# Kernel optimization log

Measured on AMD Instinct MI355X. Metric: run time of the kernel, lower is better.

## Reference

```python
import jax, jax.numpy as jnp
import numpy as np

N_EMBD = 2048
N_HEAD = 16
HEAD_DIM = N_EMBD // N_HEAD
BATCH = 2
SEQ = 2048


def setup_inputs() -> dict:
    key = jax.random.key(0)
    k1, k2, k3 = jax.random.split(key, 3)
    scale = 0.02
    return {
        "hidden_states": jax.random.normal(k1, (BATCH, SEQ, N_EMBD), dtype=jnp.float32),
        "c_attn_w": jax.random.normal(k2, (N_EMBD, 3 * N_EMBD), dtype=jnp.float32) * scale,
        "c_attn_b": jnp.zeros((3 * N_EMBD,), dtype=jnp.float32),
        "c_proj_w": jax.random.normal(k3, (N_EMBD, N_EMBD), dtype=jnp.float32) * scale,
        "c_proj_b": jnp.zeros((N_EMBD,), dtype=jnp.float32),
    }


def reference(hidden_states, c_attn_w, c_attn_b, c_proj_w, c_proj_b):
    B, S, E = hidden_states.shape
    # Fused QKV projection (Conv1D: x @ W + b)
    qkv = hidden_states @ c_attn_w + c_attn_b  # [B, S, 3E]
    q, k, v = jnp.split(qkv, 3, axis=-1)
    # split heads -> [B, H, S, D]
    def split_heads(t):
        return t.reshape(B, S, N_HEAD, HEAD_DIM).transpose(0, 2, 1, 3)
    q, k, v = split_heads(q), split_heads(k), split_heads(v)
    # scaled scores, causal mask, softmax (dropout p=0 -> identity)
    scores = jnp.einsum("bhqd,bhkd->bhqk", q, k) / jnp.asarray(
        HEAD_DIM ** 0.5, dtype=q.dtype)
    causal = jnp.tril(jnp.ones((S, S), dtype=bool))  # [S, S]
    mask_value = jnp.finfo(scores.dtype).min
    scores = jnp.where(causal[None, None, :, :], scores, mask_value)
    attn = jax.nn.softmax(scores, axis=-1)
    out = jnp.einsum("bhqk,bhkd->bhqd", attn, v)  # [B, H, S, D]
    # merge heads -> [B, S, E]
    out = out.transpose(0, 2, 1, 3).reshape(B, S, E)
    # output projection
    return out @ c_proj_w + c_proj_b
```

## Files before the change

### kernel.cpp

```cpp
#include <hip/hip_runtime.h>
#include <hip/hip_bf16.h>

typedef __bf16 bf16x8 __attribute__((ext_vector_type(8)));
typedef float f32x4 __attribute__((ext_vector_type(4)));
typedef unsigned short us4 __attribute__((ext_vector_type(4)));
typedef unsigned short us8 __attribute__((ext_vector_type(8)));

__device__ __forceinline__ float bf2f(unsigned short u) {
  union { unsigned int i; float f; } v; v.i = ((unsigned int)u) << 16; return v.f;
}
__device__ __forceinline__ unsigned short f2bf(float f) {
  union { unsigned int i; float f; } v; v.f = f;
  unsigned int i = v.i;
  return (unsigned short)((i + 0x7FFFu + ((i >> 16) & 1u)) >> 16);
}

typedef const __attribute__((address_space(1))) unsigned int* gas_ptr;
typedef __attribute__((address_space(3))) unsigned int* las_ptr;
__device__ __forceinline__ void gload_lds16(const unsigned short* g, unsigned short* l) {
  __builtin_amdgcn_global_load_lds((gas_ptr)(const void*)g, (las_ptr)(void*)l, 16, 0, 0);
}

__global__ __launch_bounds__(256) void detect_k(const unsigned short* __restrict__ h,
                                                int* __restrict__ flag) {
  __shared__ int s[256];
  int cnt = 0;
  for (int i = threadIdx.x; i < 4096; i += 256) {
    unsigned short u = h[2 * i];
    int e = (u >> 7) & 0xFF;
    if ((e >= 96 && e <= 140) || u == 0) cnt++;
  }
  s[threadIdx.x] = cnt;
  __syncthreads();
  for (int o = 128; o > 0; o >>= 1) {
    if (threadIdx.x < o) s[threadIdx.x] += s[threadIdx.x + o];
    __syncthreads();
  }
  if (threadIdx.x == 0) *flag = (s[0] >= 3600) ? 1 : 0;
}

__global__ __launch_bounds__(256) void cvt_hidden_k(const void* __restrict__ src,
                                                    unsigned short* __restrict__ dst, int n8,
                                                    const int* __restrict__ flag) {
  if (*flag) return;
  const float4* s = (const float4*)src;
  for (int i = blockIdx.x * 256 + threadIdx.x; i < n8; i += gridDim.x * 256) {
    float4 a = s[2 * i], b = s[2 * i + 1];
    us8 o;
    o[0] = f2bf(a.x); o[1] = f2bf(a.y); o[2] = f2bf(a.z); o[3] = f2bf(a.w);
    o[4] = f2bf(b.x); o[5] = f2bf(b.y); o[6] = f2bf(b.z); o[7] = f2bf(b.w);
    *(us8*)&dst[8 * i] = o;
  }
}

__global__ __launch_bounds__(256) void transpose_w2_k(const void* __restrict__ w_qkv,
                                                      const void* __restrict__ w_proj,
                                                      unsigned short* __restrict__ dst_qkv,
                                                      unsigned short* __restrict__ dst_proj,
                                                      const int* __restrict__ flag) {
  __shared__ unsigned short tile[32][33];
  const int f = *flag;
  int bid = blockIdx.x;
  const void* src;
  unsigned short* dst;
  int R = 2048, C, cx, cy;
  if (bid < 12288) {
    src = w_qkv; dst = dst_qkv; C = 6144; cx = bid % 192; cy = bid / 192;
  } else {
    bid -= 12288;
    src = w_proj; dst = dst_proj; C = 2048; cx = bid % 64; cy = bid / 64;
  }
  const int x = threadIdx.x & 31;
  const int y = threadIdx.x >> 5;
  const int r0 = cy * 32, c0 = cx * 32;
#pragma unroll
  for (int i = 0; i < 4; i++) {
    size_t idx = (size_t)(r0 + y + 8 * i) * C + c0 + x;
    tile[y + 8 * i][x] = f ? ((const unsigned short*)src)[idx]
                           : f2bf(((const float*)src)[idx]);
  }
  __syncthreads();
  const int orow = threadIdx.x >> 3;
  const int oc = (threadIdx.x & 7) * 4;
  us4 v;
  v[0] = tile[oc][orow]; v[1] = tile[oc + 1][orow];
  v[2] = tile[oc + 2][orow]; v[3] = tile[oc + 3][orow];
  *(us4*)&dst[(size_t)(c0 + orow) * R + r0 + oc] = v;
}

__global__ __launch_bounds__(256) void transpose_v_k(const unsigned short* __restrict__ qkv,
                                                     unsigned short* __restrict__ Vt) {
  __shared__ unsigned short tile[32][33];
  const int bh = blockIdx.z;
  const int b = bh >> 4, hh = bh & 15;
  const int s0 = blockIdx.x * 32, d0 = blockIdx.y * 32;
  const int x = threadIdx.x & 31, y = threadIdx.x >> 5;
#pragma unroll
  for (int i = 0; i < 4; i++)
    tile[y + 8 * i][x] =
        qkv[((size_t)b * 2048 + s0 + y + 8 * i) * 6144 + 4096 + hh * 128 + d0 + x];
  __syncthreads();
#pragma unroll
  for (int i = 0; i < 4; i++)
    Vt[((size_t)bh * 128 + d0 + y + 8 * i) * 2048 + s0 + x] = tile[x][y + 8 * i];
}

__global__ __launch_bounds__(512, 2) void gemm_qkv_k(const unsigned short* __restrict__ A_bf,
                                                     const unsigned short* __restrict__ A_cvt,
                                                     const unsigned short* __restrict__ Bt,
                                                     const void* __restrict__ bias,
                                                     unsigned short* __restrict__ Cout,
                                                     int M, int N, int K,
                                                     const int* __restrict__ flag) {
  __shared__ __attribute__((aligned(16))) unsigned short As[2][256][64];
  __shared__ __attribute__((aligned(16))) unsigned short Bs[2][192][64];
  const int f = *flag;
  const unsigned short* Ap = f ? A_bf : A_cvt;
  const int t = threadIdx.x;
  const int wave = t >> 6, lane = t & 63;
  const int col = lane & 15, quad = lane >> 4;
  const int wm = wave >> 1, wn = wave & 1;

  const int nbx = N / 192;
  int wgid = blockIdx.y * nbx + blockIdx.x;
  const int nwg = (M >> 8) * nbx;
  if ((nwg & 7) == 0) {
    const int cpx = nwg >> 3;
    wgid = (wgid & 7) * cpx + (wgid >> 3);
  }
  const int n0 = (wgid % nbx) * 192;
  const int m0 = (wgid / nbx) << 8;

  const int srow = lane >> 3;
  const int sx = ((lane & 7) ^ srow) * 8;
  const int rsw = col & 7;

  const unsigned short* pA = Ap + (size_t)(m0 + wave * 8 + srow) * K + sx;
  const unsigned short* pB = Bt + (size_t)(n0 + wave * 8 + srow) * K + sx;
  const int NT = K >> 6;

#define STAGE_A(d, q, kt) \
  gload_lds16(pA + (size_t)((q) * 64) * K + (size_t)(kt) * 64, &As[(d)][(q) * 64 + wave * 8][0])
#define STAGE_B(d, q, kt) \
  gload_lds16(pB + (size_t)((q) * 64) * K + (size_t)(kt) * 64, &Bs[(d)][(q) * 64 + wave * 8][0])
#define LDA(d, rf, kk) \
  (*(const bf16x8*)&As[(d)][wm * 64 + (rf) * 16 + col][((((kk) << 2) | quad) ^ rsw) * 8])
#define LDB(d, cf, kk) \
  (*(const bf16x8*)&Bs[(d)][wn * 96 + (cf) * 16 + col][((((kk) << 2) | quad) ^ rsw) * 8])

  const f32x4 fzero = {0.f, 0.f, 0.f, 0.f};
  f32x4 acc[4][6];
#pragma unroll
  for (int i = 0; i < 4; i++)
#pragma unroll
    for (int j = 0; j < 6; j++) acc[i][j] = fzero;

  bf16x8 aA[4][2], aB[4][2];

  STAGE_A(0, 0, 0); STAGE_A(0, 1, 0); STAGE_A(0, 2, 0); STAGE_A(0, 3, 0);
  STAGE_B(0, 0, 0); STAGE_B(0, 1, 0); STAGE_B(0, 2, 0);
  STAGE_A(1, 0, 1); STAGE_A(1, 1, 1); STAGE_A(1, 2, 1); STAGE_A(1, 3, 1);
  asm volatile("s_waitcnt vmcnt(4)" ::: "memory");
  __builtin_amdgcn_sched_barrier(0);
  __builtin_amdgcn_s_barrier();

#define BODY(D, U, FIRST, SB, SA, VM2, VM3, PRER, ACUR, ANXT)                              \
  {                                                                                        \
    if (FIRST) {                                                                           \
      _Pragma("unroll") for (int rf = 0; rf < 4; rf++) {                                   \
        ACUR[rf][0] = LDA(D, rf, 0);                                                       \
        ACUR[rf][1] = LDA(D, rf, 1);                                                       \
      }                                                                                    \
    }                                                                                      \
    bf16x8 b01[2][2];                                                                      \
    _Pragma("unroll") for (int c = 0; c < 2; c++) {                                        \
      b01[c][0] = LDB(D, c, 0);                                                            \
      b01[c][1] = LDB(D, c, 1);                                                            \
    }                                                                                      \
    if (SB) { STAGE_B((D) ^ 1, 0, (U) + 1); STAGE_B((D) ^ 1, 1, (U) + 1); }                \
    __builtin_amdgcn_s_barrier();                                                          \
    asm volatile("s_waitcnt lgkmcnt(0)" ::: "memory");                                     \
    __builtin_amdgcn_sched_barrier(0);                                                     \
    __builtin_amdgcn_s_setprio(1);                                                         \
    _Pragma("unroll") for (int rf = 0; rf < 4; rf++)                                       \
      _Pragma("unroll") for (int c = 0; c < 2; c++) {                                      \
        acc[rf][c] = __builtin_amdgcn_mfma_f32_16x16x32_bf16(ACUR[rf][0], b01[c][0], acc[rf][c], 0, 0, 0); \
        acc[rf][c] = __builtin_amdgcn_mfma_f32_16x16x32_bf16(ACUR[rf][1], b01[c][1], acc[rf][c], 0, 0, 0); \
      }                                                                                    \
    __builtin_amdgcn_s_setprio(0);                                                         \
    bf16x8 b23[2][2];                                                                      \
    _Pragma("unroll") for (int c = 0; c < 2; c++) {                                        \
      b23[c][0] = LDB(D, (c) + 2, 0);                                                      \
      b23[c][1] = LDB(D, (c) + 2, 1);                                                      \
    }                                                                                      \
    if (SB) STAGE_B((D) ^ 1, 2, (U) + 1);                                                  \
    if (SA) { STAGE_A(D, 0, (U) + 2); STAGE_A(D, 1, (U) + 2); }                            \
    asm volatile("s_waitcnt " VM2 ::: "memory");                                           \
    __builtin_amdgcn_s_barrier();                                                          \
    asm volatile("s_waitcnt lgkmcnt(0)" ::: "memory");                                     \
    __builtin_amdgcn_sched_barrier(0);                                                     \
    __builtin_amdgcn_s_setprio(1);                                                         \
    _Pragma("unroll") for (int rf = 0; rf < 4; rf++)                                       \
      _Pragma("unroll") for (int c = 0; c < 2; c++) {                                      \
        acc[rf][(c) + 2] = __builtin_amdgcn_mfma_f32_16x16x32_bf16(ACUR[rf][0], b23[c][0], acc[rf][(c) + 2], 0, 0, 0); \
        acc[rf][(c) + 2] = __builtin_amdgcn_mfma_f32_16x16x32_bf16(ACUR[rf][1], b23[c][1], acc[rf][(c) + 2], 0, 0, 0); \
      }                                                                                    \
    __builtin_amdgcn_s_setprio(0);                                                         \
    bf16x8 b45[2][2];                                                                      \
    _Pragma("unroll") for (int c = 0; c < 2; c++) {                                        \
      b45[c][0] = LDB(D, (c) + 4, 0);                                                      \
      b45[c][1] = LDB(D, (c) + 4, 1);                                                      \
    }                                                                                      \
    __builtin_amdgcn_sched_barrier(0);  \
    if (PRER) {                                                                            \
      _Pragma("unroll") for (int rf = 0; rf < 4; rf++) {                                   \
        ANXT[rf][0] = LDA((D) ^ 1, rf, 0);                                                 \
        ANXT[rf][1] = LDA((D) ^ 1, rf, 1);                                                 \
      }                                                                                    \
    }                                                                                      \
    if (SA) { STAGE_A(D, 2, (U) + 2); STAGE_A(D, 3, (U) + 2); }                            \
    asm volatile("s_waitcnt " VM3 ::: "memory");                                           \
    __builtin_amdgcn_s_barrier();                                                          \
    if (PRER) asm volatile("s_waitcnt lgkmcnt(8)" ::: "memory");                           \
    else      asm volatile("s_waitcnt lgkmcnt(0)" ::: "memory");                           \
    __builtin_amdgcn_sched_barrier(0);                                                     \
    __builtin_amdgcn_s_setprio(1);                                                         \
    _Pragma("unroll") for (int rf = 0; rf < 4; rf++)                                       \
      _Pragma("unroll") for (int c = 0; c < 2; c++) {                                      \
        acc[rf][(c) + 4] = __builtin_amdgcn_mfma_f32_16x16x32_bf16(ACUR[rf][0], b45[c][0], acc[rf][(c) + 4], 0, 0, 0); \
        acc[rf][(c) + 4] = __builtin_amdgcn_mfma_f32_16x16x32_bf16(ACUR[rf][1], b45[c][1], acc[rf][(c) + 4], 0, 0, 0); \
      }                                                                                    \
    __builtin_amdgcn_s_setprio(0);                                                         \
  }

  BODY(0, 0, 1, 1, 1, "vmcnt(5)", "vmcnt(4)", 1, aA, aB)
  BODY(1, 1, 0, 1, 1, "vmcnt(5)", "vmcnt(4)", 1, aB, aA)
  for (int u2 = 2; u2 + 3 < NT; u2 += 2) {
    BODY(0, u2, 0, 1, 1, "vmcnt(5)", "vmcnt(4)", 1, aA, aB)
    BODY(1, u2 + 1, 0, 1, 1, "vmcnt(5)", "vmcnt(4)", 1, aB, aA)
  }
  BODY(0, NT - 2, 0, 1, 0, "vmcnt(3)", "vmcnt(0)", 1, aA, aB)
  BODY(1, NT - 1, 0, 0, 0, "vmcnt(0)", "vmcnt(0)", 0, aB, aA)

#undef BODY
#undef STAGE_A
#undef STAGE_B
#undef LDA
#undef LDB

#pragma unroll
  for (int cf = 0; cf < 6; cf++) {
    int n = n0 + wn * 96 + cf * 16 + col;
    float bv = f ? bf2f(((const unsigned short*)bias)[n]) : ((const float*)bias)[n];
#pragma unroll
    for (int rf = 0; rf < 4; rf++)
#pragma unroll
      for (int r = 0; r < 4; r++) {
        int m = m0 + wm * 64 + rf * 16 + quad * 4 + r;
        Cout[(size_t)m * N + n] = f2bf(acc[rf][cf][r] + bv);
      }
  }
}

__global__ __launch_bounds__(512, 2) void gemm_proj_k(const unsigned short* __restrict__ A,
                                                      const unsigned short* __restrict__ Bt,
                                                      const void* __restrict__ bias,
                                                      void* __restrict__ Cout,
                                                      int M, int N, int K,
                                                      const int* __restrict__ flag) {
  __shared__ __attribute__((aligned(16))) unsigned short As[2][256][64];
  __shared__ __attribute__((aligned(16))) unsigned short Bs[2][128][64];
  const int f = *flag;
  const int t = threadIdx.x;
  const int wave = t >> 6, lane = t & 63;
  const int col = lane & 15, quad = lane >> 4;
  const int wm = wave >> 1, wn = wave & 1;

  const int nbx = N >> 7;
  int wgid = blockIdx.y * nbx + blockIdx.x;
  const int nwg = (M >> 8) * nbx;
  if ((nwg & 7) == 0) {
    const int cpx = nwg >> 3;
    wgid = (wgid & 7) * cpx + (wgid >> 3);
  }
  const int n0 = (wgid % nbx) << 7;
  const int m0 = (wgid / nbx) << 8;

  const int srow = lane >> 3;
  const int sx = ((lane & 7) ^ srow) * 8;
  const int rsw = col & 7;

  const unsigned short* pA = A + (size_t)(m0 + wave * 8 + srow) * K + sx;
  const unsigned short* pB = Bt + (size_t)(n0 + wave * 8 + srow) * K + sx;
  const int NT = K >> 6;

#define STAGE_A(d, q, kt) \
  gload_lds16(pA + (size_t)((q) * 64) * K + (size_t)(kt) * 64, &As[(d)][(q) * 64 + wave * 8][0])
#define STAGE_B(d, q, kt) \
  gload_lds16(pB + (size_t)((q) * 64) * K + (size_t)(kt) * 64, &Bs[(d)][(q) * 64 + wave * 8][0])
#define LDA(d, rf, kk) \
  (*(const bf16x8*)&As[(d)][wm * 64 + (rf) * 16 + col][((((kk) << 2) | quad) ^ rsw) * 8])
#define LDB(d, cf, kk) \
  (*(const bf16x8*)&Bs[(d)][wn * 64 + (cf) * 16 + col][((((kk) << 2) | quad) ^ rsw) * 8])

  const f32x4 fzero = {0.f, 0.f, 0.f, 0.f};
  f32x4 acc[4][4];
#pragma unroll
  for (int i = 0; i < 4; i++)
#pragma unroll
    for (int j = 0; j < 4; j++) acc[i][j] = fzero;

  bf16x8 aA[4][2], aB[4][2];

  STAGE_A(0, 0, 0); STAGE_A(0, 1, 0); STAGE_A(0, 2, 0); STAGE_A(0, 3, 0);
  STAGE_B(0, 0, 0); STAGE_B(0, 1, 0);
  STAGE_A(1, 0, 1); STAGE_A(1, 1, 1); STAGE_A(1, 2, 1); STAGE_A(1, 3, 1);
  asm volatile("s_waitcnt vmcnt(4)" ::: "memory");
  __builtin_amdgcn_sched_barrier(0);
  __builtin_amdgcn_s_barrier();

#define BODY(D, U, FIRST, SB, SA, VM1, VM2, PRER, ACUR, ANXT)                              \
  {                                                                                        \
    if (FIRST) {                                                                           \
      _Pragma("unroll") for (int rf = 0; rf < 4; rf++) {                                   \
        ACUR[rf][0] = LDA(D, rf, 0);                                                       \
        ACUR[rf][1] = LDA(D, rf, 1);                                                       \
      }                                                                                    \
    }                                                                                      \
    bf16x8 b01[2][2];                                                                      \
    _Pragma("unroll") for (int c = 0; c < 2; c++) {                                        \
      b01[c][0] = LDB(D, c, 0);                                                            \
      b01[c][1] = LDB(D, c, 1);                                                            \
    }                                                                                      \
    if (SB) { STAGE_B((D) ^ 1, 0, (U) + 1); STAGE_B((D) ^ 1, 1, (U) + 1); }                \
    asm volatile("s_waitcnt " VM1 ::: "memory");                                           \
    __builtin_amdgcn_s_barrier();                                                          \
    asm volatile("s_waitcnt lgkmcnt(0)" ::: "memory");                                     \
    __builtin_amdgcn_sched_barrier(0);                                                     \
    __builtin_amdgcn_s_setprio(1);                                                         \
    _Pragma("unroll") for (int rf = 0; rf < 4; rf++)                                       \
      _Pragma("unroll") for (int c = 0; c < 2; c++) {                                      \
        acc[rf][c] = __builtin_amdgcn_mfma_f32_16x16x32_bf16(ACUR[rf][0], b01[c][0], acc[rf][c], 0, 0, 0); \
        acc[rf][c] = __builtin_amdgcn_mfma_f32_16x16x32_bf16(ACUR[rf][1], b01[c][1], acc[rf][c], 0, 0, 0); \
      }                                                                                    \
    __builtin_amdgcn_s_setprio(0);                                                         \
    bf16x8 b23[2][2];                                                                      \
    _Pragma("unroll") for (int c = 0; c < 2; c++) {                                        \
      b23[c][0] = LDB(D, (c) + 2, 0);                                                      \
      b23[c][1] = LDB(D, (c) + 2, 1);                                                      \
    }                                                                                      \
    __builtin_amdgcn_sched_barrier(0);                      \
    if (PRER) {                                                                            \
      _Pragma("unroll") for (int rf = 0; rf < 4; rf++) {                                   \
        ANXT[rf][0] = LDA((D) ^ 1, rf, 0);                                                 \
        ANXT[rf][1] = LDA((D) ^ 1, rf, 1);                                                 \
      }                                                                                    \
    }                                                                                      \
    if (SA) { STAGE_A(D, 0, (U) + 2); STAGE_A(D, 1, (U) + 2);                              \
              STAGE_A(D, 2, (U) + 2); STAGE_A(D, 3, (U) + 2); }                            \
    asm volatile("s_waitcnt " VM2 ::: "memory");                                           \
    __builtin_amdgcn_s_barrier();                                                          \
    if (PRER) asm volatile("s_waitcnt lgkmcnt(8)" ::: "memory");                           \
    else      asm volatile("s_waitcnt lgkmcnt(0)" ::: "memory");                           \
    __builtin_amdgcn_sched_barrier(0);                                                     \
    __builtin_amdgcn_s_setprio(1);                                                         \
    _Pragma("unroll") for (int rf = 0; rf < 4; rf++)                                       \
      _Pragma("unroll") for (int c = 0; c < 2; c++) {                                      \
        acc[rf][(c) + 2] = __builtin_amdgcn_mfma_f32_16x16x32_bf16(ACUR[rf][0], b23[c][0], acc[rf][(c) + 2], 0, 0, 0); \
        acc[rf][(c) + 2] = __builtin_amdgcn_mfma_f32_16x16x32_bf16(ACUR[rf][1], b23[c][1], acc[rf][(c) + 2], 0, 0, 0); \
      }                                                                                    \
    __builtin_amdgcn_s_setprio(0);                                                         \
  }

  BODY(0, 0, 1, 1, 1, "vmcnt(2)", "vmcnt(4)", 1, aA, aB)
  BODY(1, 1, 0, 1, 1, "vmcnt(2)", "vmcnt(4)", 1, aB, aA)
  for (int u2 = 2; u2 + 3 < NT; u2 += 2) {
    BODY(0, u2, 0, 1, 1, "vmcnt(2)", "vmcnt(4)", 1, aA, aB)
    BODY(1, u2 + 1, 0, 1, 1, "vmcnt(2)", "vmcnt(4)", 1, aB, aA)
  }
  BODY(0, NT - 2, 0, 1, 0, "vmcnt(2)", "vmcnt(0)", 1, aA, aB)
  BODY(1, NT - 1, 0, 0, 0, "vmcnt(0)", "vmcnt(0)", 0, aB, aA)

#undef BODY
#undef STAGE_A
#undef STAGE_B
#undef LDA
#undef LDB

  const int f32o = (f == 0);
#pragma unroll
  for (int cf = 0; cf < 4; cf++) {
    int n = n0 + wn * 64 + cf * 16 + col;
    float bv = f ? bf2f(((const unsigned short*)bias)[n]) : ((const float*)bias)[n];
#pragma unroll
    for (int rf = 0; rf < 4; rf++)
#pragma unroll
      for (int r = 0; r < 4; r++) {
        int m = m0 + wm * 64 + rf * 16 + quad * 4 + r;
        float v = acc[rf][cf][r] + bv;
        if (f32o) ((float*)Cout)[(size_t)m * N + n] = v;
        else      ((unsigned short*)Cout)[(size_t)m * N + n] = f2bf(v);
      }
  }
}

#define ATT_SCALE 0.08838834764831845f
__global__ __launch_bounds__(256) void attn_k(const unsigned short* __restrict__ qkv,
                                              const unsigned short* __restrict__ Vt,
                                              unsigned short* __restrict__ O) {
  __shared__ __attribute__((aligned(16))) unsigned short Ks[64][136];
  __shared__ __attribute__((aligned(16))) unsigned short Vs[128][72];
  __shared__ __attribute__((aligned(16))) unsigned short Ps[4][16][72];
  const int t = threadIdx.x;
  const int wave = t >> 6, lane = t & 63;
  const int col = lane & 15, quad = lane >> 4;
  const int h = blockIdx.y, b = blockIdx.z;
  const size_t base = (size_t)b * 2048 * 6144;
  const size_t vbase = ((size_t)(b * 16 + h)) * 128 * 2048;
  const int hcol = h * 128;

  const int kr = t >> 2;
  const int kc = (t & 3) * 8;
  const int vr = t >> 1;
  const int vc = (t & 1) * 32;

  const f32x4 fzero = {0.f, 0.f, 0.f, 0.f};

  for (int pass = 0; pass < 2; pass++) {
    const int qt = pass ? (int)blockIdx.x : 31 - (int)blockIdx.x;

    bf16x8 qf[4];
    {
      size_t qrow = base + (size_t)(qt * 64 + wave * 16 + col) * 6144 + hcol;
#pragma unroll
      for (int ks = 0; ks < 4; ks++)
        qf[ks] = *(const bf16x8*)&qkv[qrow + ks * 32 + quad * 8];
    }

    f32x4 o[8];
#pragma unroll
    for (int i = 0; i < 8; i++) o[i] = fzero;
    float l_i[4] = {0.f, 0.f, 0.f, 0.f};

    __syncthreads();
    {
      size_t grow = base + (size_t)kr * 6144 + 2048 + hcol;
#pragma unroll
      for (int p = 0; p < 4; p++)
        *(bf16x8*)&Ks[kr][kc + p * 32] = *(const bf16x8*)&qkv[grow + kc + p * 32];
      size_t vrow = vbase + (size_t)vr * 2048;
#pragma unroll
      for (int c = 0; c < 4; c++)
        *(bf16x8*)&Vs[vr][vc + c * 8] = *(const bf16x8*)&Vt[vrow + vc + c * 8];
    }
    __syncthreads();

    for (int kt = 0; kt <= qt; kt++) {
      bf16x8 kreg[4], vreg[4];
      const bool pf = (kt < qt);
      if (pf) {
        size_t grow = base + (size_t)((kt + 1) * 64 + kr) * 6144 + 2048 + hcol;
#pragma unroll
        for (int p = 0; p < 4; p++)
          kreg[p] = *(const bf16x8*)&qkv[grow + kc + p * 32];
        size_t vrow = vbase + (size_t)vr * 2048 + (kt + 1) * 64;
#pragma unroll
        for (int c = 0; c < 4; c++)
          vreg[c] = *(const bf16x8*)&Vt[vrow + vc + c * 8];
      }

      f32x4 sc[4];
      __builtin_amdgcn_s_setprio(1);
#pragma unroll
      for (int nb = 0; nb < 4; nb++) {
        f32x4 s = fzero;
#pragma unroll
        for (int ks = 0; ks < 4; ks++) {
          bf16x8 kf = *(const bf16x8*)&Ks[nb * 16 + col][ks * 32 + quad * 8];
          s = __builtin_amdgcn_mfma_f32_16x16x32_bf16(qf[ks], kf, s, 0, 0, 0);
        }
        sc[nb] = s;
      }
      __builtin_amdgcn_s_setprio(0);

      const bool diag = (kt == qt);
#pragma unroll
      for (int nb = 0; nb < 4; nb++) {
        int kl = nb * 16 + col;
#pragma unroll
        for (int r = 0; r < 4; r++) {
          float s = sc[nb][r];
          if (diag && kl > wave * 16 + quad * 4 + r) s = -1e30f;
          float p = __expf(s * ATT_SCALE);
          l_i[r] += p;
          Ps[wave][quad * 4 + r][nb * 16 + col] = f2bf(p);
        }
      }
      bf16x8 pfr[2];
#pragma unroll
      for (int ks2 = 0; ks2 < 2; ks2++)
        pfr[ks2] = *(const bf16x8*)&Ps[wave][col][ks2 * 32 + quad * 8];
      __builtin_amdgcn_s_setprio(1);
#pragma unroll
      for (int nbo = 0; nbo < 8; nbo++)
#pragma unroll
        for (int ks2 = 0; ks2 < 2; ks2++) {
          bf16x8 vf = *(const bf16x8*)&Vs[nbo * 16 + col][ks2 * 32 + quad * 8];
          o[nbo] = __builtin_amdgcn_mfma_f32_16x16x32_bf16(pfr[ks2], vf, o[nbo], 0, 0, 0);
        }
      __builtin_amdgcn_s_setprio(0);

      __syncthreads();
      if (pf) {
#pragma unroll
        for (int p = 0; p < 4; p++)
          *(bf16x8*)&Ks[kr][kc + p * 32] = kreg[p];
#pragma unroll
        for (int c = 0; c < 4; c++)
          *(bf16x8*)&Vs[vr][vc + c * 8] = vreg[c];
      }
      __syncthreads();
    }

#pragma unroll
    for (int r = 0; r < 4; r++) {
#pragma unroll
      for (int off = 1; off < 16; off <<= 1)
        l_i[r] += __shfl_xor(l_i[r], off, 64);
      l_i[r] = 1.0f / l_i[r];
    }

#pragma unroll
    for (int nbo = 0; nbo < 8; nbo++)
#pragma unroll
      for (int r = 0; r < 4; r++) {
        int m = qt * 64 + wave * 16 + quad * 4 + r;
        O[((size_t)b * 2048 + m) * 2048 + hcol + nbo * 16 + col] = f2bf(o[nbo][r] * l_i[r]);
      }
  }
}

extern "C" void kernel_launch(void* const* d_in, const int* in_sizes, int n_in,
                              void* d_out, int out_size, void* d_ws, size_t ws_size,
                              hipStream_t stream) {
  (void)in_sizes; (void)n_in; (void)out_size; (void)ws_size;
  int* flag = (int*)d_ws;
  unsigned short* wsu = (unsigned short*)d_ws + 128;
  unsigned short* Wt_qkv    = wsu;
  unsigned short* Wt_proj   = Wt_qkv + (size_t)6144 * 2048;
  unsigned short* QKV       = Wt_proj + (size_t)2048 * 2048;
  unsigned short* hidden_bf = QKV + (size_t)4096 * 6144;
  unsigned short* Obuf      = Wt_qkv;
  unsigned short* Vt        = hidden_bf + (size_t)4096 * 2048;

  detect_k<<<1, 256, 0, stream>>>((const unsigned short*)d_in[0], flag);
  cvt_hidden_k<<<2048, 256, 0, stream>>>(d_in[0], hidden_bf, (4096 * 2048) / 8, flag);
  transpose_w2_k<<<16384, 256, 0, stream>>>(d_in[1], d_in[3], Wt_qkv, Wt_proj, flag);
  gemm_qkv_k<<<dim3(32, 16), 512, 0, stream>>>((const unsigned short*)d_in[0], hidden_bf,
                                               Wt_qkv, d_in[2], QKV,
                                               4096, 6144, 2048, flag);
  transpose_v_k<<<dim3(64, 4, 32), 256, 0, stream>>>(QKV, Vt);
  attn_k<<<dim3(16, 16, 2), 256, 0, stream>>>(QKV, Vt, Obuf);
  gemm_proj_k<<<dim3(16, 16), 512, 0, stream>>>(Obuf, Wt_proj, d_in[4], d_out,
                                                4096, 2048, 2048, flag);
}
```

Measured before the change: 385.0 us.

## Double-buffer attention K/V tiles and reschedule GEMM LDS/global staging

The attention kernel now keeps two LDS buffers for K and V, so the next tile is written into the alternate buffer and one of the two per-iteration block barriers goes away. The softmax exponent switches from __expf with a natural-log scale to exp2f with a log2e-folded scale. In the GEMM body, all B staging is issued earlier and the A-fragment prefetch for the next stage is split across two barrier phases with adjusted lgkmcnt waits. The double buffer doubles the K/V LDS footprint, which may reduce occupancy.

```diff
diff --git a/kernel.cpp b/kernel.cpp
--- a/kernel.cpp
+++ b/kernel.cpp
@@ -166,6 +166,7 @@
 
 #define BODY(D, U, FIRST, SB, SA, VM2, VM3, PRER, ACUR, ANXT)                              \
   {                                                                                        \
+                                                  \
     if (FIRST) {                                                                           \
       _Pragma("unroll") for (int rf = 0; rf < 4; rf++) {                                   \
         ACUR[rf][0] = LDA(D, rf, 0);                                                       \
@@ -177,7 +178,8 @@
       b01[c][0] = LDB(D, c, 0);                                                            \
       b01[c][1] = LDB(D, c, 1);                                                            \
     }                                                                                      \
-    if (SB) { STAGE_B((D) ^ 1, 0, (U) + 1); STAGE_B((D) ^ 1, 1, (U) + 1); }                \
+    if (SB) { STAGE_B((D) ^ 1, 0, (U) + 1); STAGE_B((D) ^ 1, 1, (U) + 1);                  \
+              STAGE_B((D) ^ 1, 2, (U) + 1); }                                              \
     __builtin_amdgcn_s_barrier();                                                          \
     asm volatile("s_waitcnt lgkmcnt(0)" ::: "memory");                                     \
     __builtin_amdgcn_sched_barrier(0);                                                     \
@@ -188,16 +190,26 @@
         acc[rf][c] = __builtin_amdgcn_mfma_f32_16x16x32_bf16(ACUR[rf][1], b01[c][1], acc[rf][c], 0, 0, 0); \
       }                                                                                    \
     __builtin_amdgcn_s_setprio(0);                                                         \
+                                                  \
     bf16x8 b23[2][2];                                                                      \
     _Pragma("unroll") for (int c = 0; c < 2; c++) {                                        \
       b23[c][0] = LDB(D, (c) + 2, 0);                                                      \
       b23[c][1] = LDB(D, (c) + 2, 1);                                                      \
     }                                                                                      \
-    if (SB) STAGE_B((D) ^ 1, 2, (U) + 1);                                                  \
     if (SA) { STAGE_A(D, 0, (U) + 2); STAGE_A(D, 1, (U) + 2); }                            \
     asm volatile("s_waitcnt " VM2 ::: "memory");                                           \
+    __builtin_amdgcn_sched_barrier(0);                                                     \
     __builtin_amdgcn_s_barrier();                                                          \
-    asm volatile("s_waitcnt lgkmcnt(0)" ::: "memory");                                     \
+    __builtin_amdgcn_sched_barrier(0);                                                     \
+    if (PRER) {                                                                            \
+      _Pragma("unroll") for (int rf = 0; rf < 2; rf++) {                                   \
+        ANXT[rf][0] = LDA((D) ^ 1, rf, 0);                                                 \
+        ANXT[rf][1] = LDA((D) ^ 1, rf, 1);                                                 \
+      }                                                                                    \
+      asm volatile("s_waitcnt lgkmcnt(4)" ::: "memory");                                   \
+    } else {                                                                               \
+      asm volatile("s_waitcnt lgkmcnt(0)" ::: "memory");                                   \
+    }                                                                                      \
     __builtin_amdgcn_sched_barrier(0);                                                     \
     __builtin_amdgcn_s_setprio(1);                                                         \
     _Pragma("unroll") for (int rf = 0; rf < 4; rf++)                                       \
@@ -206,23 +218,26 @@
         acc[rf][(c) + 2] = __builtin_amdgcn_mfma_f32_16x16x32_bf16(ACUR[rf][1], b23[c][1], acc[rf][(c) + 2], 0, 0, 0); \
       }                                                                                    \
     __builtin_amdgcn_s_setprio(0);                                                         \
+                                                  \
     bf16x8 b45[2][2];                                                                      \
     _Pragma("unroll") for (int c = 0; c < 2; c++) {                                        \
       b45[c][0] = LDB(D, (c) + 4, 0);                                                      \
       b45[c][1] = LDB(D, (c) + 4, 1);                                                      \
     }                                                                                      \
-    __builtin_amdgcn_sched_barrier(0);  \
+    if (SA) { STAGE_A(D, 2, (U) + 2); STAGE_A(D, 3, (U) + 2); }                            \
+    asm volatile("s_waitcnt " VM3 ::: "memory");                                           \
+    __builtin_amdgcn_sched_barrier(0);                                                     \
+    __builtin_amdgcn_s_barrier();                                                          \
+    __builtin_amdgcn_sched_barrier(0);                                                     \
     if (PRER) {                                                                            \
-      _Pragma("unroll") for (int rf = 0; rf < 4; rf++) {                                   \
+      _Pragma("unroll") for (int rf = 2; rf < 4; rf++) {                                   \
         ANXT[rf][0] = LDA((D) ^ 1, rf, 0);                                                 \
         ANXT[rf][1] = LDA((D) ^ 1, rf, 1);                                                 \
       }                                                                                    \
-    }                                                                                      \
-    if (SA) { STAGE_A(D, 2, (U) + 2); STAGE_A(D, 3, (U) + 2); }                            \
-    asm volatile("s_waitcnt " VM3 ::: "memory");                                           \
-    __builtin_amdgcn_s_barrier();                                                          \
-    if (PRER) asm volatile("s_waitcnt lgkmcnt(8)" ::: "memory");                           \
-    else      asm volatile("s_waitcnt lgkmcnt(0)" ::: "memory");                           \
+      asm volatile("s_waitcnt lgkmcnt(4)" ::: "memory");                                   \
+    } else {                                                                               \
+      asm volatile("s_waitcnt lgkmcnt(0)" ::: "memory");                                   \
+    }                                                                                      \
     __builtin_amdgcn_sched_barrier(0);                                                     \
     __builtin_amdgcn_s_setprio(1);                                                         \
     _Pragma("unroll") for (int rf = 0; rf < 4; rf++)                                       \
@@ -404,12 +419,12 @@
   }
 }
 
-#define ATT_SCALE 0.08838834764831845f
+#define ATT_SC2 0.1275174367076458f
 __global__ __launch_bounds__(256) void attn_k(const unsigned short* __restrict__ qkv,
                                               const unsigned short* __restrict__ Vt,
                                               unsigned short* __restrict__ O) {
-  __shared__ __attribute__((aligned(16))) unsigned short Ks[64][136];
-  __shared__ __attribute__((aligned(16))) unsigned short Vs[128][72];
+  __shared__ __attribute__((aligned(16))) unsigned short Ks[2][64][136];
+  __shared__ __attribute__((aligned(16))) unsigned short Vs[2][128][72];
   __shared__ __attribute__((aligned(16))) unsigned short Ps[4][16][72];
   const int t = threadIdx.x;
   const int wave = t >> 6, lane = t & 63;
@@ -447,13 +462,14 @@
       size_t grow = base + (size_t)kr * 6144 + 2048 + hcol;
 #pragma unroll
       for (int p = 0; p < 4; p++)
-        *(bf16x8*)&Ks[kr][kc + p * 32] = *(const bf16x8*)&qkv[grow + kc + p * 32];
+        *(bf16x8*)&Ks[0][kr][kc + p * 32] = *(const bf16x8*)&qkv[grow + kc + p * 32];
       size_t vrow = vbase + (size_t)vr * 2048;
 #pragma unroll
       for (int c = 0; c < 4; c++)
-        *(bf16x8*)&Vs[vr][vc + c * 8] = *(const bf16x8*)&Vt[vrow + vc + c * 8];
+        *(bf16x8*)&Vs[0][vr][vc + c * 8] = *(const bf16x8*)&Vt[vrow + vc + c * 8];
     }
     __syncthreads();
+    int dbf = 0;
 
     for (int kt = 0; kt <= qt; kt++) {
       bf16x8 kreg[4], vreg[4];
@@ -476,7 +492,7 @@
         f32x4 s = fzero;
 #pragma unroll
         for (int ks = 0; ks < 4; ks++) {
-          bf16x8 kf = *(const bf16x8*)&Ks[nb * 16 + col][ks * 32 + quad * 8];
+          bf16x8 kf = *(const bf16x8*)&Ks[dbf][nb * 16 + col][ks * 32 + quad * 8];
           s = __builtin_amdgcn_mfma_f32_16x16x32_bf16(qf[ks], kf, s, 0, 0, 0);
         }
         sc[nb] = s;
@@ -491,7 +507,7 @@
         for (int r = 0; r < 4; r++) {
           float s = sc[nb][r];
           if (diag && kl > wave * 16 + quad * 4 + r) s = -1e30f;
-          float p = __expf(s * ATT_SCALE);
+          float p = exp2f(s * ATT_SC2);
           l_i[r] += p;
           Ps[wave][quad * 4 + r][nb * 16 + col] = f2bf(p);
         }
@@ -505,21 +521,21 @@
       for (int nbo = 0; nbo < 8; nbo++)
 #pragma unroll
         for (int ks2 = 0; ks2 < 2; ks2++) {
-          bf16x8 vf = *(const bf16x8*)&Vs[nbo * 16 + col][ks2 * 32 + quad * 8];
+          bf16x8 vf = *(const bf16x8*)&Vs[dbf][nbo * 16 + col][ks2 * 32 + quad * 8];
           o[nbo] = __builtin_amdgcn_mfma_f32_16x16x32_bf16(pfr[ks2], vf, o[nbo], 0, 0, 0);
         }
       __builtin_amdgcn_s_setprio(0);
 
+      if (pf) {
+#pragma unroll
+        for (int p = 0; p < 4; p++)
+          *(bf16x8*)&Ks[dbf ^ 1][kr][kc + p * 32] = kreg[p];
+#pragma unroll
+        for (int c = 0; c < 4; c++)
+          *(bf16x8*)&Vs[dbf ^ 1][vr][vc + c * 8] = vreg[c];
+      }
       __syncthreads();
-      if (pf) {
-#pragma unroll
-        for (int p = 0; p < 4; p++)
-          *(bf16x8*)&Ks[kr][kc + p * 32] = kreg[p];
-#pragma unroll
-        for (int c = 0; c < 4; c++)
-          *(bf16x8*)&Vs[vr][vc + c * 8] = vreg[c];
-      }
-      __syncthreads();
+      dbf ^= 1;
     }
 
 #pragma unroll
```

Result: slower. 409.5 us (+6.4%).

## Double-buffer K/V LDS tiles in attention and use exp2 with packed bf16 converts

Applied to the files above, without the earlier changes.

The attention kernel now keeps two LDS buffers for K and V. Prefetched registers go into the alternate buffer, so each iteration needs one barrier instead of two. The softmax uses exp2f with a log2e-folded scale and packs pairs of probabilities with v_cvt_pk_bf16_f32 in place of software rounding. The extra buffers roughly double K/V LDS use, which may lower occupancy, and the hardware convert may round slightly differently from the software path.

```diff
diff --git a/kernel.cpp b/kernel.cpp
--- a/kernel.cpp
+++ b/kernel.cpp
@@ -13,6 +13,11 @@
   union { unsigned int i; float f; } v; v.f = f;
   unsigned int i = v.i;
   return (unsigned short)((i + 0x7FFFu + ((i >> 16) & 1u)) >> 16);
+}
+__device__ __forceinline__ unsigned int cvtpk_bf16(float lo, float hi) {
+  unsigned int r;
+  asm("v_cvt_pk_bf16_f32 %0, %1, %2" : "=v"(r) : "v"(lo), "v"(hi));
+  return r;
 }
 
 typedef const __attribute__((address_space(1))) unsigned int* gas_ptr;
@@ -404,12 +409,12 @@
   }
 }
 
-#define ATT_SCALE 0.08838834764831845f
+#define ATT_SC2 0.1275174367076458f
 __global__ __launch_bounds__(256) void attn_k(const unsigned short* __restrict__ qkv,
                                               const unsigned short* __restrict__ Vt,
                                               unsigned short* __restrict__ O) {
-  __shared__ __attribute__((aligned(16))) unsigned short Ks[64][136];
-  __shared__ __attribute__((aligned(16))) unsigned short Vs[128][72];
+  __shared__ __attribute__((aligned(16))) unsigned short Ks[2][64][136];
+  __shared__ __attribute__((aligned(16))) unsigned short Vs[2][128][72];
   __shared__ __attribute__((aligned(16))) unsigned short Ps[4][16][72];
   const int t = threadIdx.x;
   const int wave = t >> 6, lane = t & 63;
@@ -447,13 +452,14 @@
       size_t grow = base + (size_t)kr * 6144 + 2048 + hcol;
 #pragma unroll
       for (int p = 0; p < 4; p++)
-        *(bf16x8*)&Ks[kr][kc + p * 32] = *(const bf16x8*)&qkv[grow + kc + p * 32];
+        *(bf16x8*)&Ks[0][kr][kc + p * 32] = *(const bf16x8*)&qkv[grow + kc + p * 32];
       size_t vrow = vbase + (size_t)vr * 2048;
 #pragma unroll
       for (int c = 0; c < 4; c++)
-        *(bf16x8*)&Vs[vr][vc + c * 8] = *(const bf16x8*)&Vt[vrow + vc + c * 8];
+        *(bf16x8*)&Vs[0][vr][vc + c * 8] = *(const bf16x8*)&Vt[vrow + vc + c * 8];
     }
     __syncthreads();
+    int dbf = 0;
 
     for (int kt = 0; kt <= qt; kt++) {
       bf16x8 kreg[4], vreg[4];
@@ -476,7 +482,7 @@
         f32x4 s = fzero;
 #pragma unroll
         for (int ks = 0; ks < 4; ks++) {
-          bf16x8 kf = *(const bf16x8*)&Ks[nb * 16 + col][ks * 32 + quad * 8];
+          bf16x8 kf = *(const bf16x8*)&Ks[dbf][nb * 16 + col][ks * 32 + quad * 8];
           s = __builtin_amdgcn_mfma_f32_16x16x32_bf16(qf[ks], kf, s, 0, 0, 0);
         }
         sc[nb] = s;
@@ -487,14 +493,27 @@
 #pragma unroll
       for (int nb = 0; nb < 4; nb++) {
         int kl = nb * 16 + col;
-#pragma unroll
-        for (int r = 0; r < 4; r++) {
-          float s = sc[nb][r];
-          if (diag && kl > wave * 16 + quad * 4 + r) s = -1e30f;
-          float p = __expf(s * ATT_SCALE);
-          l_i[r] += p;
-          Ps[wave][quad * 4 + r][nb * 16 + col] = f2bf(p);
+        float p0, p1, p2, p3;
+        {
+          float s0 = sc[nb][0], s1 = sc[nb][1], s2 = sc[nb][2], s3 = sc[nb][3];
+          if (diag) {
+            int qrow = wave * 16 + quad * 4;
+            if (kl > qrow + 0) s0 = -1e30f;
+            if (kl > qrow + 1) s1 = -1e30f;
+            if (kl > qrow + 2) s2 = -1e30f;
+            if (kl > qrow + 3) s3 = -1e30f;
+          }
+          p0 = exp2f(s0 * ATT_SC2); p1 = exp2f(s1 * ATT_SC2);
+          p2 = exp2f(s2 * ATT_SC2); p3 = exp2f(s3 * ATT_SC2);
+          l_i[0] += p0; l_i[1] += p1; l_i[2] += p2; l_i[3] += p3;
         }
+        unsigned int w01 = cvtpk_bf16(p0, p1);
+        unsigned int w23 = cvtpk_bf16(p2, p3);
+        unsigned short* pb = &Ps[wave][quad * 4][nb * 16 + col];
+        pb[0]   = (unsigned short)w01;
+        pb[72]  = (unsigned short)(w01 >> 16);
+        pb[144] = (unsigned short)w23;
+        pb[216] = (unsigned short)(w23 >> 16);
       }
       bf16x8 pfr[2];
 #pragma unroll
@@ -505,21 +524,21 @@
       for (int nbo = 0; nbo < 8; nbo++)
 #pragma unroll
         for (int ks2 = 0; ks2 < 2; ks2++) {
-          bf16x8 vf = *(const bf16x8*)&Vs[nbo * 16 + col][ks2 * 32 + quad * 8];
+          bf16x8 vf = *(const bf16x8*)&Vs[dbf][nbo * 16 + col][ks2 * 32 + quad * 8];
           o[nbo] = __builtin_amdgcn_mfma_f32_16x16x32_bf16(pfr[ks2], vf, o[nbo], 0, 0, 0);
         }
       __builtin_amdgcn_s_setprio(0);
 
+      if (pf) {
+#pragma unroll
+        for (int p = 0; p < 4; p++)
+          *(bf16x8*)&Ks[dbf ^ 1][kr][kc + p * 32] = kreg[p];
+#pragma unroll
+        for (int c = 0; c < 4; c++)
+          *(bf16x8*)&Vs[dbf ^ 1][vr][vc + c * 8] = vreg[c];
+      }
       __syncthreads();
-      if (pf) {
-#pragma unroll
-        for (int p = 0; p < 4; p++)
-          *(bf16x8*)&Ks[kr][kc + p * 32] = kreg[p];
-#pragma unroll
-        for (int c = 0; c < 4; c++)
-          *(bf16x8*)&Vs[vr][vc + c * 8] = vreg[c];
-      }
-      __syncthreads();
+      dbf ^= 1;
     }
 
 #pragma unroll
```

After: 378.9 us. About the same (-1.6%).

## Fuse V transpose into QKV GEMM epilogue and double-buffer attention K/V tiles

Applied to the files above, without the earlier changes.

The QKV GEMM epilogue now writes the V third of its output directly in transposed [b,h,d,s] layout, which removes the separate transpose_v_k kernel and its extra read and write of V. The attention kernel gets double-buffered K/V shared-memory tiles with a two-ahead register prefetch and one barrier per iteration, so loads overlap compute. It also uses exp2 with a folded scale, packed bf16 conversion for P, and a remapped block-to-(batch,head,qtile) order meant to improve L2 locality. The trade-offs are twice the shared memory for K/V, which can lower occupancy, and more live registers.

```diff
diff --git a/kernel.cpp b/kernel.cpp
--- a/kernel.cpp
+++ b/kernel.cpp
@@ -13,6 +13,11 @@
   union { unsigned int i; float f; } v; v.f = f;
   unsigned int i = v.i;
   return (unsigned short)((i + 0x7FFFu + ((i >> 16) & 1u)) >> 16);
+}
+__device__ __forceinline__ unsigned int cvtpk_bf16(float lo, float hi) {
+  unsigned int r;
+  asm("v_cvt_pk_bf16_f32 %0, %1, %2" : "=v"(r) : "v"(lo), "v"(hi));
+  return r;
 }
 
 typedef const __attribute__((address_space(1))) unsigned int* gas_ptr;
@@ -88,28 +93,12 @@
   *(us4*)&dst[(size_t)(c0 + orow) * R + r0 + oc] = v;
 }
 
-__global__ __launch_bounds__(256) void transpose_v_k(const unsigned short* __restrict__ qkv,
-                                                     unsigned short* __restrict__ Vt) {
-  __shared__ unsigned short tile[32][33];
-  const int bh = blockIdx.z;
-  const int b = bh >> 4, hh = bh & 15;
-  const int s0 = blockIdx.x * 32, d0 = blockIdx.y * 32;
-  const int x = threadIdx.x & 31, y = threadIdx.x >> 5;
-#pragma unroll
-  for (int i = 0; i < 4; i++)
-    tile[y + 8 * i][x] =
-        qkv[((size_t)b * 2048 + s0 + y + 8 * i) * 6144 + 4096 + hh * 128 + d0 + x];
-  __syncthreads();
-#pragma unroll
-  for (int i = 0; i < 4; i++)
-    Vt[((size_t)bh * 128 + d0 + y + 8 * i) * 2048 + s0 + x] = tile[x][y + 8 * i];
-}
-
 __global__ __launch_bounds__(512, 2) void gemm_qkv_k(const unsigned short* __restrict__ A_bf,
                                                      const unsigned short* __restrict__ A_cvt,
                                                      const unsigned short* __restrict__ Bt,
                                                      const void* __restrict__ bias,
                                                      unsigned short* __restrict__ Cout,
+                                                     unsigned short* __restrict__ Vt,
                                                      int M, int N, int K,
                                                      const int* __restrict__ flag) {
   __shared__ __attribute__((aligned(16))) unsigned short As[2][256][64];
@@ -248,17 +237,30 @@
 #undef LDA
 #undef LDB
 
+  const int vb = m0 >> 11;
+  const int vs = (m0 & 2047) + wm * 64 + quad * 4;
 #pragma unroll
   for (int cf = 0; cf < 6; cf++) {
     int n = n0 + wn * 96 + cf * 16 + col;
     float bv = f ? bf2f(((const unsigned short*)bias)[n]) : ((const float*)bias)[n];
-#pragma unroll
-    for (int rf = 0; rf < 4; rf++)
-#pragma unroll
-      for (int r = 0; r < 4; r++) {
-        int m = m0 + wm * 64 + rf * 16 + quad * 4 + r;
-        Cout[(size_t)m * N + n] = f2bf(acc[rf][cf][r] + bv);
+    if (n < 4096) {
+#pragma unroll
+      for (int rf = 0; rf < 4; rf++)
+#pragma unroll
+        for (int r = 0; r < 4; r++) {
+          int m = m0 + wm * 64 + rf * 16 + quad * 4 + r;
+          Cout[(size_t)m * N + n] = f2bf(acc[rf][cf][r] + bv);
+        }
+    } else {
+      size_t vrow = ((size_t)(vb * 2048 + (n - 4096))) * 2048;
+#pragma unroll
+      for (int rf = 0; rf < 4; rf++) {
+        us4 vv;
+#pragma unroll
+        for (int r = 0; r < 4; r++) vv[r] = f2bf(acc[rf][cf][r] + bv);
+        *(us4*)&Vt[vrow + vs + rf * 16] = vv;
       }
+    }
   }
 }
 
@@ -404,17 +406,23 @@
   }
 }
 
-#define ATT_SCALE 0.08838834764831845f
+#define ATT_SC2 0.1275174367076458f
 __global__ __launch_bounds__(256) void attn_k(const unsigned short* __restrict__ qkv,
                                               const unsigned short* __restrict__ Vt,
                                               unsigned short* __restrict__ O) {
-  __shared__ __attribute__((aligned(16))) unsigned short Ks[64][136];
-  __shared__ __attribute__((aligned(16))) unsigned short Vs[128][72];
+  __shared__ __attribute__((aligned(16))) unsigned short Ks[2][64][136];
+  __shared__ __attribute__((aligned(16))) unsigned short Vs[2][128][72];
   __shared__ __attribute__((aligned(16))) unsigned short Ps[4][16][72];
   const int t = threadIdx.x;
   const int wave = t >> 6, lane = t & 63;
   const int col = lane & 15, quad = lane >> 4;
-  const int h = blockIdx.y, b = blockIdx.z;
+
+  const int p = (int)(blockIdx.x + 16 * blockIdx.y + (blockIdx.z << 8));
+  const int j = p >> 3;
+  const int g = (p & 7) * 4 + (j >> 4);
+  const int qx = j & 15;
+  const int b = g >> 4, h = g & 15;
+
   const size_t base = (size_t)b * 2048 * 6144;
   const size_t vbase = ((size_t)(b * 16 + h)) * 128 * 2048;
   const int hcol = h * 128;
@@ -426,8 +434,79 @@
 
   const f32x4 fzero = {0.f, 0.f, 0.f, 0.f};
 
+#define LOADR(KR, VR, ktn)                                                      \
+  do {                                                                          \
+    size_t grow = base + (size_t)((ktn) * 64 + kr) * 6144 + 2048 + hcol;        \
+    _Pragma("unroll") for (int pq = 0; pq < 4; pq++)                            \
+      KR[pq] = *(const bf16x8*)&qkv[grow + kc + pq * 32];                       \
+    size_t vrow = vbase + (size_t)vr * 2048 + (ktn) * 64;                       \
+    _Pragma("unroll") for (int c = 0; c < 4; c++)                               \
+      VR[c] = *(const bf16x8*)&Vt[vrow + vc + c * 8];                           \
+  } while (0)
+
+#define ITER(KT, DBF, CK, CV, NK, NV)                                           \
+  {                                                                             \
+    if ((KT) + 2 <= qt) LOADR(NK, NV, (KT) + 2);                                \
+    f32x4 sc[4];                                                                \
+    __builtin_amdgcn_s_setprio(1);                                              \
+    _Pragma("unroll") for (int nb = 0; nb < 4; nb++) {                          \
+      f32x4 s = fzero;                                                          \
+      _Pragma("unroll") for (int ks = 0; ks < 4; ks++) {                        \
+        bf16x8 kf = *(const bf16x8*)&Ks[DBF][nb * 16 + col][ks * 32 + quad * 8];\
+        s = __builtin_amdgcn_mfma_f32_16x16x32_bf16(qf[ks], kf, s, 0, 0, 0);    \
+      }                                                                         \
+      sc[nb] = s;                                                               \
+    }                                                                           \
+    __builtin_amdgcn_s_setprio(0);                                              \
+    const bool diag = ((KT) == qt);                                             \
+    _Pragma("unroll") for (int nb = 0; nb < 4; nb++) {                          \
+      int kl = nb * 16 + col;                                                   \
+      float p0, p1, p2, p3;                                                     \
+      {                                                                         \
+        float s0 = sc[nb][0], s1 = sc[nb][1], s2 = sc[nb][2], s3 = sc[nb][3];   \
+        if (diag) {                                                             \
+          int qrow = wave * 16 + quad * 4;                                      \
+          if (kl > qrow + 0) s0 = -1e30f;                                       \
+          if (kl > qrow + 1) s1 = -1e30f;                                       \
+          if (kl > qrow + 2) s2 = -1e30f;                                       \
+          if (kl > qrow + 3) s3 = -1e30f;                                       \
+        }                                                                       \
+        p0 = exp2f(s0 * ATT_SC2); p1 = exp2f(s1 * ATT_SC2);                     \
+        p2 = exp2f(s2 * ATT_SC2); p3 = exp2f(s3 * ATT_SC2);                     \
+        l_i[0] += p0; l_i[1] += p1; l_i[2] += p2; l_i[3] += p3;                 \
+      }                                                                         \
+      unsigned int w01 = cvtpk_bf16(p0, p1);                                    \
+      unsigned int w23 = cvtpk_bf16(p2, p3);                                    \
+      unsigned short* pb = &Ps[wave][quad * 4][nb * 16 + col];                  \
+      pb[0]   = (unsigned short)w01;                                            \
+      pb[72]  = (unsigned short)(w01 >> 16);                                    \
+      pb[144] = (unsigned short)w23;                                            \
+      pb[216] = (unsigned short)(w23 >> 16);                                    \
+    }                                                                           \
+    bf16x8 pfr[2];                                                              \
+    _Pragma("unroll") for (int ks2 = 0; ks2 < 2; ks2++)                         \
+      pfr[ks2] = *(const bf16x8*)&Ps[wave][col][ks2 * 32 + quad * 8];           \
+    __builtin_amdgcn_s_setprio(1);                                              \
+    _Pragma("unroll") for (int nbo = 0; nbo < 8; nbo++)                         \
+      _Pragma("unroll") for (int ks2 = 0; ks2 < 2; ks2++) {                     \
+        bf16x8 vf = *(const bf16x8*)&Vs[DBF][nbo * 16 + col][ks2 * 32 + quad * 8]; \
+        o[nbo] = __builtin_amdgcn_mfma_f32_16x16x32_bf16(pfr[ks2], vf, o[nbo], 0, 0, 0); \
+      }                                                                         \
+    __builtin_amdgcn_s_setprio(0);                                              \
+    if ((KT) + 1 <= qt) {                                                       \
+      _Pragma("unroll") for (int pq = 0; pq < 4; pq++)                          \
+        *(bf16x8*)&Ks[(DBF) ^ 1][kr][kc + pq * 32] = CK[pq];                    \
+      _Pragma("unroll") for (int c = 0; c < 4; c++)                             \
+        *(bf16x8*)&Vs[(DBF) ^ 1][vr][vc + c * 8] = CV[c];                       \
+    }                                                                           \
+    asm volatile("s_waitcnt lgkmcnt(0)" ::: "memory");                          \
+    __builtin_amdgcn_sched_barrier(0);                                          \
+    __builtin_amdgcn_s_barrier();                                               \
+    asm volatile("" ::: "memory");                                              \
+  }
+
   for (int pass = 0; pass < 2; pass++) {
-    const int qt = pass ? (int)blockIdx.x : 31 - (int)blockIdx.x;
+    const int qt = pass ? qx : 31 - qx;
 
     bf16x8 qf[4];
     {
@@ -446,80 +525,24 @@
     {
       size_t grow = base + (size_t)kr * 6144 + 2048 + hcol;
 #pragma unroll
-      for (int p = 0; p < 4; p++)
-        *(bf16x8*)&Ks[kr][kc + p * 32] = *(const bf16x8*)&qkv[grow + kc + p * 32];
+      for (int pq = 0; pq < 4; pq++)
+        *(bf16x8*)&Ks[0][kr][kc + pq * 32] = *(const bf16x8*)&qkv[grow + kc + pq * 32];
       size_t vrow = vbase + (size_t)vr * 2048;
 #pragma unroll
       for (int c = 0; c < 4; c++)
-        *(bf16x8*)&Vs[vr][vc + c * 8] = *(const bf16x8*)&Vt[vrow + vc + c * 8];
+        *(bf16x8*)&Vs[0][vr][vc + c * 8] = *(const bf16x8*)&Vt[vrow + vc + c * 8];
     }
     __syncthreads();
 
-    for (int kt = 0; kt <= qt; kt++) {
-      bf16x8 kreg[4], vreg[4];
-      const bool pf = (kt < qt);
-      if (pf) {
-        size_t grow = base + (size_t)((kt + 1) * 64 + kr) * 6144 + 2048 + hcol;
-#pragma unroll
-        for (int p = 0; p < 4; p++)
-          kreg[p] = *(const bf16x8*)&qkv[grow + kc + p * 32];
-        size_t vrow = vbase + (size_t)vr * 2048 + (kt + 1) * 64;
-#pragma unroll
-        for (int c = 0; c < 4; c++)
-          vreg[c] = *(const bf16x8*)&Vt[vrow + vc + c * 8];
-      }
-
-      f32x4 sc[4];
-      __builtin_amdgcn_s_setprio(1);
-#pragma unroll
-      for (int nb = 0; nb < 4; nb++) {
-        f32x4 s = fzero;
-#pragma unroll
-        for (int ks = 0; ks < 4; ks++) {
-          bf16x8 kf = *(const bf16x8*)&Ks[nb * 16 + col][ks * 32 + quad * 8];
-          s = __builtin_amdgcn_mfma_f32_16x16x32_bf16(qf[ks], kf, s, 0, 0, 0);
-        }
-        sc[nb] = s;
-      }
-      __builtin_amdgcn_s_setprio(0);
-
-      const bool diag = (kt == qt);
-#pragma unroll
-      for (int nb = 0; nb < 4; nb++) {
-        int kl = nb * 16 + col;
-#pragma unroll
-        for (int r = 0; r < 4; r++) {
-          float s = sc[nb][r];
-          if (diag && kl > wave * 16 + quad * 4 + r) s = -1e30f;
-          float p = __expf(s * ATT_SCALE);
-          l_i[r] += p;
-          Ps[wave][quad * 4 + r][nb * 16 + col] = f2bf(p);
-        }
-      }
-      bf16x8 pfr[2];
-#pragma unroll
-      for (int ks2 = 0; ks2 < 2; ks2++)
-        pfr[ks2] = *(const bf16x8*)&Ps[wave][col][ks2 * 32 + quad * 8];
-      __builtin_amdgcn_s_setprio(1);
-#pragma unroll
-      for (int nbo = 0; nbo < 8; nbo++)
-#pragma unroll
-        for (int ks2 = 0; ks2 < 2; ks2++) {
-          bf16x8 vf = *(const bf16x8*)&Vs[nbo * 16 + col][ks2 * 32 + quad * 8];
-          o[nbo] = __builtin_amdgcn_mfma_f32_16x16x32_bf16(pfr[ks2], vf, o[nbo], 0, 0, 0);
-        }
-      __builtin_amdgcn_s_setprio(0);
-
-      __syncthreads();
-      if (pf) {
-#pragma unroll
-        for (int p = 0; p < 4; p++)
-          *(bf16x8*)&Ks[kr][kc + p * 32] = kreg[p];
-#pragma unroll
-        for (int c = 0; c < 4; c++)
-          *(bf16x8*)&Vs[vr][vc + c * 8] = vreg[c];
-      }
-      __syncthreads();
+    bf16x8 kA[4], vA[4], kB[4], vB[4];
+    if (qt >= 1) LOADR(kA, vA, 1);
+
+    for (int kt = 0; kt <= qt;) {
+      ITER(kt, 0, kA, vA, kB, vB);
+      kt++;
+      if (kt > qt) break;
+      ITER(kt, 1, kB, vB, kA, vA);
+      kt++;
     }
 
 #pragma unroll
@@ -538,6 +561,8 @@
         O[((size_t)b * 2048 + m) * 2048 + hcol + nbo * 16 + col] = f2bf(o[nbo][r] * l_i[r]);
       }
   }
+#undef ITER
+#undef LOADR
 }
 
 extern "C" void kernel_launch(void* const* d_in, const int* in_sizes, int n_in,
@@ -557,9 +582,8 @@
   cvt_hidden_k<<<2048, 256, 0, stream>>>(d_in[0], hidden_bf, (4096 * 2048) / 8, flag);
   transpose_w2_k<<<16384, 256, 0, stream>>>(d_in[1], d_in[3], Wt_qkv, Wt_proj, flag);
   gemm_qkv_k<<<dim3(32, 16), 512, 0, stream>>>((const unsigned short*)d_in[0], hidden_bf,
-                                               Wt_qkv, d_in[2], QKV,
+                                               Wt_qkv, d_in[2], QKV, Vt,
                                                4096, 6144, 2048, flag);
-  transpose_v_k<<<dim3(64, 4, 32), 256, 0, stream>>>(QKV, Vt);
   attn_k<<<dim3(16, 16, 2), 256, 0, stream>>>(QKV, Vt, Obuf);
   gemm_proj_k<<<dim3(16, 16), 512, 0, stream>>>(Obuf, Wt_proj, d_in[4], d_out,
                                                 4096, 2048, 2048, flag);
```

After: 401.3 us. +4.2%, slower.
